# Kernel optimization log

Measured on AMD Instinct MI355X. Metric: run time of the kernel, lower is better.

## Reference

```python
import jax, jax.numpy as jnp
import numpy as np

G = 8          # group (window) size -> N = G*G = 64
HEADS = 8
DIM = 256
HEAD_DIM = DIM // HEADS
SCALE = HEAD_DIM ** -0.5
POS_DIM = (DIM // 4) // 4  # 16
LN_EPS = 1e-5


def _make_bias_tables():
    # biases: coordinates (1-g..g-1) x (1-g..g-1) -> [(2g-1)^2, 2] float
    r = np.arange(1 - G, G)
    bh, bw = np.meshgrid(r, r, indexing='ij')
    biases = np.stack([bh.ravel(), bw.ravel()], axis=1).astype(np.float32)
    # relative position index [g^2, g^2]
    ch, cw = np.meshgrid(np.arange(G), np.arange(G), indexing='ij')
    coords = np.stack([ch.ravel(), cw.ravel()])              # [2, g^2]
    rel = coords[:, :, None] - coords[:, None, :]            # [2, g^2, g^2]
    rel = rel.transpose(1, 2, 0)
    rel[:, :, 0] += G - 1
    rel[:, :, 1] += G - 1
    rel[:, :, 0] *= 2 * G - 1
    rel_idx = rel.sum(-1).astype(np.int32)                   # [g^2, g^2]
    return biases, rel_idx


def setup_inputs() -> dict:
    key = jax.random.key(0)
    ks = jax.random.split(key, 8)
    B, N, C = 2048, G * G, DIM
    biases_np, rel_idx_np = _make_bias_tables()
    s = lambda fan: 1.0 / np.sqrt(fan)
    return {
        'x': jax.random.normal(ks[0], (B, N, C), jnp.float32),
        'qkv_w': jax.random.normal(ks[1], (C, 3 * C), jnp.float32) * s(C),
        'qkv_b': jnp.zeros((3 * C,), jnp.float32),
        'proj_w': jax.random.normal(ks[2], (C, C), jnp.float32) * s(C),
        'proj_b': jnp.zeros((C,), jnp.float32),
        'pos_proj_w': jax.random.normal(ks[3], (2, POS_DIM), jnp.float32) * s(2),
        'pos_proj_b': jnp.zeros((POS_DIM,), jnp.float32),
        'ln1_g': jnp.ones((POS_DIM,), jnp.float32), 'ln1_b': jnp.zeros((POS_DIM,), jnp.float32),
        'fc1_w': jax.random.normal(ks[4], (POS_DIM, POS_DIM), jnp.float32) * s(POS_DIM),
        'fc1_b': jnp.zeros((POS_DIM,), jnp.float32),
        'ln2_g': jnp.ones((POS_DIM,), jnp.float32), 'ln2_b': jnp.zeros((POS_DIM,), jnp.float32),
        'fc2_w': jax.random.normal(ks[5], (POS_DIM, POS_DIM), jnp.float32) * s(POS_DIM),
        'fc2_b': jnp.zeros((POS_DIM,), jnp.float32),
        'ln3_g': jnp.ones((POS_DIM,), jnp.float32), 'ln3_b': jnp.zeros((POS_DIM,), jnp.float32),
        'fc3_w': jax.random.normal(ks[6], (POS_DIM, HEADS), jnp.float32) * s(POS_DIM),
        'fc3_b': jnp.zeros((HEADS,), jnp.float32),
        'biases': jnp.asarray(biases_np),
        'rel_idx': jnp.asarray(rel_idx_np),
    }


def _ln(h, g, b):
    m = jnp.mean(h, -1, keepdims=True)
    v = jnp.mean((h - m) ** 2, -1, keepdims=True)
    return (h - m) * jax.lax.rsqrt(v + LN_EPS) * g + b


def reference(x, qkv_w, qkv_b, proj_w, proj_b,
              pos_proj_w, pos_proj_b,
              ln1_g, ln1_b, fc1_w, fc1_b,
              ln2_g, ln2_b, fc2_w, fc2_b,
              ln3_g, ln3_b, fc3_w, fc3_b,
              biases, rel_idx):
    B, N, C = x.shape
    # dynamic position bias MLP: [(2g-1)^2, 2] -> [(2g-1)^2, heads]
    h = biases @ pos_proj_w + pos_proj_b
    h = jax.nn.relu(_ln(h, ln1_g, ln1_b)) @ fc1_w + fc1_b
    h = jax.nn.relu(_ln(h, ln2_g, ln2_b)) @ fc2_w + fc2_b
    pos = jax.nn.relu(_ln(h, ln3_g, ln3_b)) @ fc3_w + fc3_b        # [225, H]
    rel_bias = pos[rel_idx]                                        # [N, N, H]
    rel_bias = jnp.transpose(rel_bias, (2, 0, 1))                  # [H, N, N]

    qkv = (x @ qkv_w + qkv_b).reshape(B, N, 3, HEADS, HEAD_DIM)
    qkv = jnp.transpose(qkv, (2, 0, 3, 1, 4))                      # [3, B, H, N, Dh]
    q, k, v = qkv[0] * SCALE, qkv[1], qkv[2]
    attn = jnp.einsum('bhnd,bhmd->bhnm', q, k) + rel_bias[None]    # [B, H, N, N]
    attn = jax.nn.softmax(attn, axis=-1)
    out = jnp.einsum('bhnm,bhmd->bhnd', attn, v)                   # [B, H, N, Dh]
    out = jnp.transpose(out, (0, 2, 1, 3)).reshape(B, N, C)
    return out @ proj_w + proj_b
```

## Files before the change

kernel.cpp:

```cpp
#include <hip/hip_runtime.h>

typedef _Float16 half_t;
typedef __attribute__((ext_vector_type(8))) _Float16 half8;
typedef __attribute__((ext_vector_type(4))) _Float16 half4;
typedef __attribute__((ext_vector_type(4))) float float4v;

#define LN_EPS 1e-5f
#define QK_SCALE 0.17677669529663687f

static __device__ __forceinline__ float4v mfma16(half8 a, half8 b, float4v c) {
    return __builtin_amdgcn_mfma_f32_16x16x32_f16(a, b, c, 0, 0, 0);
}

static __device__ __forceinline__ int swzA(int row, int colByte) {
    return row * 512 + ((((colByte >> 4) ^ ((row >> 1) & 7)) << 4) | (colByte & 15));
}
static __device__ __forceinline__ int swzB(int row, int colByte) {
    return row * 64 + ((((colByte >> 4) ^ ((row >> 1) & 3)) << 4) | (colByte & 15));
}
static __device__ __forceinline__ int swzC(int row, int colByte) {
    return row * 128 + ((((colByte >> 4) ^ (row & 7)) << 4) | (colByte & 15));
}

static __device__ void ln_relu16(float* h, const float* __restrict__ g, const float* __restrict__ b) {
    float m = 0.f;
    for (int j = 0; j < 16; ++j) m += h[j];
    m *= (1.0f / 16.0f);
    float v = 0.f;
    for (int j = 0; j < 16; ++j) { float d = h[j] - m; v += d * d; }
    v *= (1.0f / 16.0f);
    float rs = rsqrtf(v + LN_EPS);
    for (int j = 0; j < 16; ++j) {
        float t = (h[j] - m) * rs * g[j] + b[j];
        h[j] = t > 0.f ? t : 0.f;
    }
}

__global__ void prep_kernel(
    const float* __restrict__ qkv_w,
    const float* __restrict__ proj_w,
    const float* __restrict__ biases,
    const float* __restrict__ pos_w, const float* __restrict__ pos_b,
    const float* __restrict__ ln1_g, const float* __restrict__ ln1_b,
    const float* __restrict__ fc1_w, const float* __restrict__ fc1_b,
    const float* __restrict__ ln2_g, const float* __restrict__ ln2_b,
    const float* __restrict__ fc2_w, const float* __restrict__ fc2_b,
    const float* __restrict__ ln3_g, const float* __restrict__ ln3_b,
    const float* __restrict__ fc3_w, const float* __restrict__ fc3_b,
    const int* __restrict__ rel_idx,
    half_t* __restrict__ wqkvT,
    half_t* __restrict__ wprojT,
    float* __restrict__ rbp)
{
    __shared__ float tile[64][65];
    __shared__ float pos_s[225][8];
    const int t = blockIdx.x;
    const int tid = threadIdx.x;

    if (t < 64) {
        const float* src; half_t* dst; int ncols, rg, cg;
        if (t < 48) { src = qkv_w;  dst = wqkvT;  ncols = 768; rg = t / 12;      cg = t % 12; }
        else        { src = proj_w; dst = wprojT; ncols = 256; rg = (t-48) >> 2; cg = (t-48) & 3; }
        const int r0 = tid >> 6, c = tid & 63;
        for (int i = 0; i < 16; ++i) {
            int r = i * 4 + r0;
            tile[r][c] = src[(rg * 64 + r) * ncols + cg * 64 + c];
        }
        __syncthreads();
        for (int i = 0; i < 16; ++i) {
            int r = i * 4 + r0;
            dst[(cg * 64 + r) * 256 + rg * 64 + c] = (half_t)tile[c][r];
        }
    } else {
        if (tid < 225) {
            float h[16], h2[16];
            float b0 = biases[tid * 2], b1 = biases[tid * 2 + 1];
            for (int j = 0; j < 16; ++j) h[j] = b0 * pos_w[j] + b1 * pos_w[16 + j] + pos_b[j];
            ln_relu16(h, ln1_g, ln1_b);
            for (int j = 0; j < 16; ++j) {
                float s = fc1_b[j];
                for (int k = 0; k < 16; ++k) s += h[k] * fc1_w[k * 16 + j];
                h2[j] = s;
            }
            ln_relu16(h2, ln2_g, ln2_b);
            for (int j = 0; j < 16; ++j) {
                float s = fc2_b[j];
                for (int k = 0; k < 16; ++k) s += h2[k] * fc2_w[k * 16 + j];
                h[j] = s;
            }
            ln_relu16(h, ln3_g, ln3_b);
            for (int j = 0; j < 8; ++j) {
                float s = fc3_b[j];
                for (int k = 0; k < 16; ++k) s += h[k] * fc3_w[k * 8 + j];
                pos_s[tid][j] = s;
            }
        }
        __syncthreads();
        for (int e = tid; e < 8 * 64 * 64; e += 256) {
            int hh = e >> 12, rem = e & 4095;
            int row = rem >> 6, c = rem & 63;
            int tj = c >> 4, mm = c & 15;
            rbp[hh * 4096 + row * 64 + mm * 4 + tj] = pos_s[rel_idx[row * 64 + c]][hh];
        }
    }
}

__global__ __launch_bounds__(256, 3) void qkv_attn_kernel(
    const float* __restrict__ x,
    const half_t* __restrict__ wqkvT,
    const float* __restrict__ qkv_b,
    const float* __restrict__ rbp,
    half_t* __restrict__ attn_ws)
{
    __shared__ __align__(16) char smem[49152];
    char* xs = smem;

    const int bb  = blockIdx.x;
    const int win = bb >> 1;
    const int tid = threadIdx.x;
    const int w    = tid >> 6;
    const int h    = (bb & 1) * 4 + w;
    const int lane = tid & 63;
    const int m = lane & 15;
    const int g = lane >> 4;
    char* wA  = smem + 32768 + w * 4096;
    char* vts = xs + w * 8192;

    const float* xg = x + (size_t)win * 16384;
    #pragma unroll
    for (int i = 0; i < 16; ++i) {
        int u = tid + i * 256;
        int row = u >> 6, c4 = u & 63;
        float4v xv = *(const float4v*)(xg + u * 4);
        half4 hv;
        hv[0] = (half_t)xv[0]; hv[1] = (half_t)xv[1];
        hv[2] = (half_t)xv[2]; hv[3] = (half_t)xv[3];
        *(half4*)(xs + swzA(row, c4 * 8)) = hv;
    }
    __syncthreads();

    float4v qb[2][2];
    #pragma unroll
    for (int pt = 0; pt < 2; ++pt)
        #pragma unroll
        for (int c2 = 0; c2 < 2; ++c2)
            qb[pt][c2] = *(const float4v*)(qkv_b + pt * 256 + h * 32 + c2 * 16 + g * 4);

    half8 aq[4], bk[4];
    {
        float4v qa[2][4], ka[2][4];
        #pragma unroll
        for (int c2 = 0; c2 < 2; ++c2)
            #pragma unroll
            for (int ti = 0; ti < 4; ++ti) {
                qa[c2][ti] = {0.f, 0.f, 0.f, 0.f};
                ka[c2][ti] = {0.f, 0.f, 0.f, 0.f};
            }
        const half_t* wqb = wqkvT + (size_t)(h * 32 + m) * 256 + g * 8;
        #pragma unroll
        for (int kk = 0; kk < 8; ++kk) {
            half8 af[4];
            #pragma unroll
            for (int ti = 0; ti < 4; ++ti)
                af[ti] = *(const half8*)(xs + swzA(ti * 16 + m, kk * 64 + g * 16));
            half8 wq0 = *(const half8*)(wqb + kk * 32);
            half8 wq1 = *(const half8*)(wqb + 16 * 256 + kk * 32);
            half8 wk0 = *(const half8*)(wqb + 256 * 256 + kk * 32);
            half8 wk1 = *(const half8*)(wqb + 272 * 256 + kk * 32);
            #pragma unroll
            for (int ti = 0; ti < 4; ++ti) {
                qa[0][ti] = mfma16(wq0, af[ti], qa[0][ti]);
                qa[1][ti] = mfma16(wq1, af[ti], qa[1][ti]);
                ka[0][ti] = mfma16(wk0, af[ti], ka[0][ti]);
                ka[1][ti] = mfma16(wk1, af[ti], ka[1][ti]);
            }
        }
        #pragma unroll
        for (int c2 = 0; c2 < 2; ++c2)
            #pragma unroll
            for (int ti = 0; ti < 4; ++ti) {
                half4 t;
                #pragma unroll
                for (int r = 0; r < 4; ++r) t[r] = (half_t)(qa[c2][ti][r] + qb[0][c2][r]);
                *(half4*)(wA + ti * 1024 + swzB(m, (c2 * 16 + g * 4) * 2)) = t;
            }
        #pragma unroll
        for (int ti = 0; ti < 4; ++ti)
            aq[ti] = *(const half8*)(wA + ti * 1024 + swzB(m, g * 16));
        __builtin_amdgcn_sched_barrier(0);
        #pragma unroll
        for (int c2 = 0; c2 < 2; ++c2)
            #pragma unroll
            for (int ti = 0; ti < 4; ++ti) {
                half4 t;
                #pragma unroll
                for (int r = 0; r < 4; ++r) t[r] = (half_t)(ka[c2][ti][r] + qb[1][c2][r]);
                *(half4*)(wA + ti * 1024 + swzB(m, (c2 * 16 + g * 4) * 2)) = t;
            }
        #pragma unroll
        for (int ti = 0; ti < 4; ++ti)
            bk[ti] = *(const half8*)(wA + ti * 1024 + swzB(m, g * 16));
        __builtin_amdgcn_sched_barrier(0);
    }

    half4 ph[4][4];
    const float* rbh = rbp + h * 4096;
    #pragma unroll
    for (int ti = 0; ti < 4; ++ti) {
        float4v z = {0.f, 0.f, 0.f, 0.f};
        float4v s0 = mfma16(aq[ti], bk[0], z);
        float4v s1 = mfma16(aq[ti], bk[1], z);
        float4v s2 = mfma16(aq[ti], bk[2], z);
        float4v s3 = mfma16(aq[ti], bk[3], z);
        #pragma unroll
        for (int r = 0; r < 4; ++r) {
            float4v rb = *(const float4v*)(rbh + (ti * 16 + g * 4 + r) * 64 + m * 4);
            float e0 = __expf(s0[r] * QK_SCALE + rb[0]);
            float e1 = __expf(s1[r] * QK_SCALE + rb[1]);
            float e2 = __expf(s2[r] * QK_SCALE + rb[2]);
            float e3 = __expf(s3[r] * QK_SCALE + rb[3]);
            float s = e0 + e1 + e2 + e3;
            s += __shfl_xor(s, 1); s += __shfl_xor(s, 2);
            s += __shfl_xor(s, 4); s += __shfl_xor(s, 8);
            float is = 1.0f / s;
            ph[ti][0][r] = (half_t)(e0 * is);
            ph[ti][1][r] = (half_t)(e1 * is);
            ph[ti][2][r] = (half_t)(e2 * is);
            ph[ti][3][r] = (half_t)(e3 * is);
        }
    }

    half4 vh[2][4];
    {
        float4v va[2][4];
        #pragma unroll
        for (int c2 = 0; c2 < 2; ++c2)
            #pragma unroll
            for (int ti = 0; ti < 4; ++ti) va[c2][ti] = {0.f, 0.f, 0.f, 0.f};
        const half_t* wvb = wqkvT + (size_t)(512 + h * 32 + m) * 256 + g * 8;
        #pragma unroll
        for (int kk = 0; kk < 8; ++kk) {
            half8 wv0 = *(const half8*)(wvb + kk * 32);
            half8 wv1 = *(const half8*)(wvb + 16 * 256 + kk * 32);
            #pragma unroll
            for (int ti = 0; ti < 4; ++ti) {
                half8 af = *(const half8*)(xs + swzA(ti * 16 + m, kk * 64 + g * 16));
                va[0][ti] = mfma16(af, wv0, va[0][ti]);
                va[1][ti] = mfma16(af, wv1, va[1][ti]);
            }
        }
        float vb0 = qkv_b[512 + h * 32 + m], vb1 = qkv_b[512 + h * 32 + 16 + m];
        #pragma unroll
        for (int c2 = 0; c2 < 2; ++c2)
            #pragma unroll
            for (int ti = 0; ti < 4; ++ti)
                #pragma unroll
                for (int r = 0; r < 4; ++r)
                    vh[c2][ti][r] = (half_t)(va[c2][ti][r] + (c2 ? vb1 : vb0));
    }
    __syncthreads();

    #pragma unroll
    for (int c2 = 0; c2 < 2; ++c2)
        #pragma unroll
        for (int ti = 0; ti < 4; ++ti)
            *(half4*)(vts + swzC(c2 * 16 + m, ti * 32 + g * 8)) = vh[c2][ti];

    float4v oacc[2][4];
    #pragma unroll
    for (int tjd = 0; tjd < 2; ++tjd)
        #pragma unroll
        for (int ti = 0; ti < 4; ++ti) oacc[tjd][ti] = {0.f, 0.f, 0.f, 0.f};
    #pragma unroll
    for (int nc = 0; nc < 2; ++nc) {
        #pragma unroll
        for (int ti = 0; ti < 4; ++ti)
            #pragma unroll
            for (int t2 = 0; t2 < 2; ++t2)
                #pragma unroll
                for (int r = 0; r < 4; ++r)
                    *(half_t*)(wA + swzB(ti * 16 + g * 4 + r, (t2 * 16 + m) * 2)) =
                        ph[ti][nc * 2 + t2][r];
        half8 pa[4];
        #pragma unroll
        for (int ti = 0; ti < 4; ++ti)
            pa[ti] = *(const half8*)(wA + swzB(ti * 16 + m, g * 16));
        #pragma unroll
        for (int tjd = 0; tjd < 2; ++tjd) {
            half8 bv = *(const half8*)(vts + swzC(tjd * 16 + m, nc * 64 + g * 16));
            #pragma unroll
            for (int ti = 0; ti < 4; ++ti)
                oacc[tjd][ti] = mfma16(pa[ti], bv, oacc[tjd][ti]);
        }
        __builtin_amdgcn_sched_barrier(0);
    }

    half_t* ag = attn_ws + (size_t)win * 16384;
    #pragma unroll
    for (int tjd = 0; tjd < 2; ++tjd)
        #pragma unroll
        for (int ti = 0; ti < 4; ++ti)
            #pragma unroll
            for (int r = 0; r < 4; ++r)
                ag[(ti * 16 + g * 4 + r) * 256 + h * 32 + tjd * 16 + m] =
                    (half_t)oacc[tjd][ti][r];
}

__global__ __launch_bounds__(256, 4) void proj_kernel(
    const half_t* __restrict__ attn_ws,
    const half_t* __restrict__ wprojT,
    const float* __restrict__ proj_b,
    float* __restrict__ out)
{
    __shared__ __align__(16) char smem[32768];
    char* xs = smem;

    const int win = blockIdx.x;
    const int tid = threadIdx.x;
    const int w    = tid >> 6;
    const int lane = tid & 63;
    const int m = lane & 15;
    const int g = lane >> 4;

    const half_t* ag = attn_ws + (size_t)win * 16384;
    #pragma unroll
    for (int i = 0; i < 8; ++i) {
        int u = tid + i * 256;
        int row = u >> 5, c8 = u & 31;
        half8 v = *(const half8*)(ag + u * 8);
        *(half8*)(xs + swzA(row, c8 * 16)) = v;
    }
    __syncthreads();

    float* og = out + (size_t)win * 16384;
    #pragma unroll
    for (int cp = 0; cp < 2; ++cp) {
        const int oc0 = w * 64 + cp * 32;
        float4v pacc[2][4];
        #pragma unroll
        for (int c2 = 0; c2 < 2; ++c2)
            #pragma unroll
            for (int ti = 0; ti < 4; ++ti) pacc[c2][ti] = {0.f, 0.f, 0.f, 0.f};
        const half_t* wpb = wprojT + (size_t)(oc0 + m) * 256 + g * 8;
        #pragma unroll
        for (int kk = 0; kk < 8; ++kk) {
            half8 wf0 = *(const half8*)(wpb + kk * 32);
            half8 wf1 = *(const half8*)(wpb + 16 * 256 + kk * 32);
            #pragma unroll
            for (int ti = 0; ti < 4; ++ti) {
                half8 af = *(const half8*)(xs + swzA(ti * 16 + m, kk * 64 + g * 16));
                pacc[0][ti] = mfma16(af, wf0, pacc[0][ti]);
                pacc[1][ti] = mfma16(af, wf1, pacc[1][ti]);
            }
        }
        float pb0 = proj_b[oc0 + m], pb1 = proj_b[oc0 + 16 + m];
        #pragma unroll
        for (int c2 = 0; c2 < 2; ++c2)
            #pragma unroll
            for (int ti = 0; ti < 4; ++ti)
                #pragma unroll
                for (int r = 0; r < 4; ++r)
                    og[(ti * 16 + g * 4 + r) * 256 + oc0 + c2 * 16 + m] =
                        pacc[c2][ti][r] + (c2 ? pb1 : pb0);
    }
}

__global__ __launch_bounds__(512, 2) void fused_fallback(
    const float* __restrict__ x,
    const half_t* __restrict__ wqkvT,
    const float* __restrict__ qkv_b,
    const half_t* __restrict__ wprojT,
    const float* __restrict__ proj_b,
    const float* __restrict__ rbp,
    float* __restrict__ out)
{
    __shared__ __align__(16) char smem[65536];
    char* xs  = smem;
    char* atn = smem;
    char* arenas = smem + 32768;

    const int b   = blockIdx.x;
    const int tid = threadIdx.x;
    const int w    = tid >> 6;
    const int lane = tid & 63;
    const int m = lane & 15;
    const int g = lane >> 4;
    char* wA  = arenas + w * 4096;
    char* vts = xs + w * 4096;

    const float* xg = x + (size_t)b * 16384;
    #pragma unroll
    for (int i = 0; i < 8; ++i) {
        int u = tid + i * 512;
        int row = u >> 6, c4 = u & 63;
        float4v xv = *(const float4v*)(xg + u * 4);
        half4 hv;
        hv[0] = (half_t)xv[0]; hv[1] = (half_t)xv[1];
        hv[2] = (half_t)xv[2]; hv[3] = (half_t)xv[3];
        *(half4*)(xs + swzA(row, c4 * 8)) = hv;
    }
    __syncthreads();

    float4v qb[2][2];
    #pragma unroll
    for (int pt = 0; pt < 2; ++pt)
        #pragma unroll
        for (int c2 = 0; c2 < 2; ++c2)
            qb[pt][c2] = *(const float4v*)(qkv_b + pt * 256 + w * 32 + c2 * 16 + g * 4);

    half8 aq[4], bk[4];
    {
        float4v qa[2][4], ka[2][4];
        #pragma unroll
        for (int c2 = 0; c2 < 2; ++c2)
            #pragma unroll
            for (int ti = 0; ti < 4; ++ti) {
                qa[c2][ti] = {0.f, 0.f, 0.f, 0.f};
                ka[c2][ti] = {0.f, 0.f, 0.f, 0.f};
            }
        const half_t* wqb = wqkvT + (size_t)(w * 32 + m) * 256 + g * 8;
        #pragma unroll
        for (int kk = 0; kk < 8; ++kk) {
            half8 af[4];
            #pragma unroll
            for (int ti = 0; ti < 4; ++ti)
                af[ti] = *(const half8*)(xs + swzA(ti * 16 + m, kk * 64 + g * 16));
            half8 wq0 = *(const half8*)(wqb + kk * 32);
            half8 wq1 = *(const half8*)(wqb + 16 * 256 + kk * 32);
            half8 wk0 = *(const half8*)(wqb + 256 * 256 + kk * 32);
            half8 wk1 = *(const half8*)(wqb + 272 * 256 + kk * 32);
            #pragma unroll
            for (int ti = 0; ti < 4; ++ti) {
                qa[0][ti] = mfma16(wq0, af[ti], qa[0][ti]);
                qa[1][ti] = mfma16(wq1, af[ti], qa[1][ti]);
                ka[0][ti] = mfma16(wk0, af[ti], ka[0][ti]);
                ka[1][ti] = mfma16(wk1, af[ti], ka[1][ti]);
            }
        }
        #pragma unroll
        for (int c2 = 0; c2 < 2; ++c2)
            #pragma unroll
            for (int ti = 0; ti < 4; ++ti) {
                half4 t;
                #pragma unroll
                for (int r = 0; r < 4; ++r) t[r] = (half_t)(qa[c2][ti][r] + qb[0][c2][r]);
                *(half4*)(wA + ti * 1024 + swzB(m, (c2 * 16 + g * 4) * 2)) = t;
            }
        #pragma unroll
        for (int ti = 0; ti < 4; ++ti)
            aq[ti] = *(const half8*)(wA + ti * 1024 + swzB(m, g * 16));
        __builtin_amdgcn_sched_barrier(0);
        #pragma unroll
        for (int c2 = 0; c2 < 2; ++c2)
            #pragma unroll
            for (int ti = 0; ti < 4; ++ti) {
                half4 t;
                #pragma unroll
                for (int r = 0; r < 4; ++r) t[r] = (half_t)(ka[c2][ti][r] + qb[1][c2][r]);
                *(half4*)(wA + ti * 1024 + swzB(m, (c2 * 16 + g * 4) * 2)) = t;
            }
        #pragma unroll
        for (int ti = 0; ti < 4; ++ti)
            bk[ti] = *(const half8*)(wA + ti * 1024 + swzB(m, g * 16));
        __builtin_amdgcn_sched_barrier(0);
    }

    half4 ph[4][4];
    const float* rbh = rbp + w * 4096;
    #pragma unroll
    for (int ti = 0; ti < 4; ++ti) {
        float4v z = {0.f, 0.f, 0.f, 0.f};
        float4v s0 = mfma16(aq[ti], bk[0], z);
        float4v s1 = mfma16(aq[ti], bk[1], z);
        float4v s2 = mfma16(aq[ti], bk[2], z);
        float4v s3 = mfma16(aq[ti], bk[3], z);
        #pragma unroll
        for (int r = 0; r < 4; ++r) {
            float4v rb = *(const float4v*)(rbh + (ti * 16 + g * 4 + r) * 64 + m * 4);
            float e0 = __expf(s0[r] * QK_SCALE + rb[0]);
            float e1 = __expf(s1[r] * QK_SCALE + rb[1]);
            float e2 = __expf(s2[r] * QK_SCALE + rb[2]);
            float e3 = __expf(s3[r] * QK_SCALE + rb[3]);
            float s = e0 + e1 + e2 + e3;
            s += __shfl_xor(s, 1); s += __shfl_xor(s, 2);
            s += __shfl_xor(s, 4); s += __shfl_xor(s, 8);
            float is = 1.0f / s;
            ph[ti][0][r] = (half_t)(e0 * is);
            ph[ti][1][r] = (half_t)(e1 * is);
            ph[ti][2][r] = (half_t)(e2 * is);
            ph[ti][3][r] = (half_t)(e3 * is);
        }
    }

    half4 vh[2][4];
    {
        float4v va[2][4];
        #pragma unroll
        for (int c2 = 0; c2 < 2; ++c2)
            #pragma unroll
            for (int ti = 0; ti < 4; ++ti) va[c2][ti] = {0.f, 0.f, 0.f, 0.f};
        const half_t* wvb = wqkvT + (size_t)(512 + w * 32 + m) * 256 + g * 8;
        #pragma unroll
        for (int kk = 0; kk < 8; ++kk) {
            half8 wv0 = *(const half8*)(wvb + kk * 32);
            half8 wv1 = *(const half8*)(wvb + 16 * 256 + kk * 32);
            #pragma unroll
            for (int ti = 0; ti < 4; ++ti) {
                half8 af = *(const half8*)(xs + swzA(ti * 16 + m, kk * 64 + g * 16));
                va[0][ti] = mfma16(af, wv0, va[0][ti]);
                va[1][ti] = mfma16(af, wv1, va[1][ti]);
            }
        }
        float vb0 = qkv_b[512 + w * 32 + m], vb1 = qkv_b[512 + w * 32 + 16 + m];
        #pragma unroll
        for (int c2 = 0; c2 < 2; ++c2)
            #pragma unroll
            for (int ti = 0; ti < 4; ++ti)
                #pragma unroll
                for (int r = 0; r < 4; ++r)
                    vh[c2][ti][r] = (half_t)(va[c2][ti][r] + (c2 ? vb1 : vb0));
    }
    __syncthreads();

    #pragma unroll
    for (int c2 = 0; c2 < 2; ++c2)
        #pragma unroll
        for (int ti = 0; ti < 4; ++ti)
            *(half4*)(vts + swzC(c2 * 16 + m, ti * 32 + g * 8)) = vh[c2][ti];

    float4v oacc[2][4];
    #pragma unroll
    for (int tjd = 0; tjd < 2; ++tjd)
        #pragma unroll
        for (int ti = 0; ti < 4; ++ti) oacc[tjd][ti] = {0.f, 0.f, 0.f, 0.f};
    #pragma unroll
    for (int nc = 0; nc < 2; ++nc) {
        #pragma unroll
        for (int ti = 0; ti < 4; ++ti)
            #pragma unroll
            for (int t2 = 0; t2 < 2; ++t2)
                #pragma unroll
                for (int r = 0; r < 4; ++r)
                    *(half_t*)(wA + swzB(ti * 16 + g * 4 + r, (t2 * 16 + m) * 2)) =
                        ph[ti][nc * 2 + t2][r];
        half8 pa[4];
        #pragma unroll
        for (int ti = 0; ti < 4; ++ti)
            pa[ti] = *(const half8*)(wA + swzB(ti * 16 + m, g * 16));
        #pragma unroll
        for (int tjd = 0; tjd < 2; ++tjd) {
            half8 bv = *(const half8*)(vts + swzC(tjd * 16 + m, nc * 64 + g * 16));
            #pragma unroll
            for (int ti = 0; ti < 4; ++ti)
                oacc[tjd][ti] = mfma16(pa[ti], bv, oacc[tjd][ti]);
        }
        __builtin_amdgcn_sched_barrier(0);
    }
    __syncthreads();

    #pragma unroll
    for (int tjd = 0; tjd < 2; ++tjd)
        #pragma unroll
        for (int ti = 0; ti < 4; ++ti)
            #pragma unroll
            for (int r = 0; r < 4; ++r)
                *(half_t*)(atn + swzA(ti * 16 + g * 4 + r, (w * 32 + tjd * 16 + m) * 2)) =
                    (half_t)oacc[tjd][ti][r];
    __syncthreads();

    float* og = out + (size_t)b * 16384;
    const int oc0 = w * 32;
    float4v pacc[2][4];
    #pragma unroll
    for (int c2 = 0; c2 < 2; ++c2)
        #pragma unroll
        for (int ti = 0; ti < 4; ++ti) pacc[c2][ti] = {0.f, 0.f, 0.f, 0.f};
    const half_t* wpb = wprojT + (size_t)(oc0 + m) * 256 + g * 8;
    #pragma unroll
    for (int kk = 0; kk < 8; ++kk) {
        half8 wf0 = *(const half8*)(wpb + kk * 32);
        half8 wf1 = *(const half8*)(wpb + 16 * 256 + kk * 32);
        #pragma unroll
        for (int ti = 0; ti < 4; ++ti) {
            half8 af = *(const half8*)(atn + swzA(ti * 16 + m, kk * 64 + g * 16));
            pacc[0][ti] = mfma16(af, wf0, pacc[0][ti]);
            pacc[1][ti] = mfma16(af, wf1, pacc[1][ti]);
        }
    }
    float pb0 = proj_b[oc0 + m], pb1 = proj_b[oc0 + 16 + m];
    #pragma unroll
    for (int c2 = 0; c2 < 2; ++c2)
        #pragma unroll
        for (int ti = 0; ti < 4; ++ti)
            #pragma unroll
            for (int r = 0; r < 4; ++r)
                og[(ti * 16 + g * 4 + r) * 256 + oc0 + c2 * 16 + m] =
                    pacc[c2][ti][r] + (c2 ? pb1 : pb0);
}

extern "C" void kernel_launch(void* const* d_in, const int* in_sizes, int n_in,
                              void* d_out, int out_size, void* d_ws, size_t ws_size,
                              hipStream_t stream) {
    const float* x          = (const float*)d_in[0];
    const float* qkv_w      = (const float*)d_in[1];
    const float* qkv_b      = (const float*)d_in[2];
    const float* proj_w     = (const float*)d_in[3];
    const float* proj_b     = (const float*)d_in[4];
    const float* pos_proj_w = (const float*)d_in[5];
    const float* pos_proj_b = (const float*)d_in[6];
    const float* ln1_g = (const float*)d_in[7];
    const float* ln1_b = (const float*)d_in[8];
    const float* fc1_w = (const float*)d_in[9];
    const float* fc1_b = (const float*)d_in[10];
    const float* ln2_g = (const float*)d_in[11];
    const float* ln2_b = (const float*)d_in[12];
    const float* fc2_w = (const float*)d_in[13];
    const float* fc2_b = (const float*)d_in[14];
    const float* ln3_g = (const float*)d_in[15];
    const float* ln3_b = (const float*)d_in[16];
    const float* fc3_w = (const float*)d_in[17];
    const float* fc3_b = (const float*)d_in[18];
    const float* biases = (const float*)d_in[19];
    const int*  rel_idx = (const int*)d_in[20];

    half_t* wqkvT  = (half_t*)d_ws;
    half_t* wprojT = (half_t*)((char*)d_ws + 393216);
    float*  rbp    = (float*)((char*)d_ws + 524288);
    half_t* attn_ws = (half_t*)((char*)d_ws + 655360);

    const int B = in_sizes[0] / (64 * 256);
    const size_t need = 655360 + (size_t)B * 64 * 256 * 2;

    prep_kernel<<<65, 256, 0, stream>>>(qkv_w, proj_w, biases, pos_proj_w, pos_proj_b,
                                        ln1_g, ln1_b, fc1_w, fc1_b,
                                        ln2_g, ln2_b, fc2_w, fc2_b,
                                        ln3_g, ln3_b, fc3_w, fc3_b,
                                        rel_idx, wqkvT, wprojT, rbp);
    if (ws_size >= need) {
        qkv_attn_kernel<<<B * 2, 256, 0, stream>>>(x, wqkvT, qkv_b, rbp, attn_ws);
        proj_kernel<<<B, 256, 0, stream>>>(attn_ws, wprojT, proj_b, (float*)d_out);
    } else {
        fused_fallback<<<B, 512, 0, stream>>>(x, wqkvT, qkv_b, wprojT, proj_b, rbp,
                                              (float*)d_out);
    }
}
```

Measured before the change: 311.5 us.

## Split fused QKV+attention into separate QKV GEMM and attention kernels

Replaces the per-head fused QKV projection and attention kernel with a per-window QKV GEMM kernel, which writes Q, K and transposed V to global scratch, followed by a separate attention kernel. The goal is to stop loading and converting x twice per window and to give the GEMM better occupancy. In exchange, Q, K and V make extra round trips through global memory, d_out is reused as temporary storage, and a larger workspace is required.

```diff
diff --git a/kernel.cpp b/kernel.cpp
--- a/kernel.cpp
+++ b/kernel.cpp
@@ -105,26 +105,19 @@
     }
 }
 
-__global__ __launch_bounds__(256, 3) void qkv_attn_kernel(
+__global__ __launch_bounds__(256, 4) void qkv_gemm_kernel(
     const float* __restrict__ x,
     const half_t* __restrict__ wqkvT,
     const float* __restrict__ qkv_b,
-    const float* __restrict__ rbp,
-    half_t* __restrict__ attn_ws)
+    half_t* __restrict__ q_ws,
+    half_t* __restrict__ k_ws,
+    half_t* __restrict__ vt_ws)
 {
-    __shared__ __align__(16) char smem[49152];
+    __shared__ __align__(16) char smem[32768];
     char* xs = smem;
-
-    const int bb  = blockIdx.x;
-    const int win = bb >> 1;
+    const int win = blockIdx.x;
     const int tid = threadIdx.x;
-    const int w    = tid >> 6;
-    const int h    = (bb & 1) * 4 + w;
-    const int lane = tid & 63;
-    const int m = lane & 15;
-    const int g = lane >> 4;
-    char* wA  = smem + 32768 + w * 4096;
-    char* vts = xs + w * 8192;
+    const int w = tid >> 6, lane = tid & 63, m = lane & 15, g = lane >> 4;
 
     const float* xg = x + (size_t)win * 16384;
     #pragma unroll
@@ -139,71 +132,81 @@
     }
     __syncthreads();
 
-    float4v qb[2][2];
-    #pragma unroll
-    for (int pt = 0; pt < 2; ++pt)
-        #pragma unroll
-        for (int c2 = 0; c2 < 2; ++c2)
-            qb[pt][c2] = *(const float4v*)(qkv_b + pt * 256 + h * 32 + c2 * 16 + g * 4);
-
-    half8 aq[4], bk[4];
-    {
-        float4v qa[2][4], ka[2][4];
-        #pragma unroll
-        for (int c2 = 0; c2 < 2; ++c2)
-            #pragma unroll
-            for (int ti = 0; ti < 4; ++ti) {
-                qa[c2][ti] = {0.f, 0.f, 0.f, 0.f};
-                ka[c2][ti] = {0.f, 0.f, 0.f, 0.f};
-            }
-        const half_t* wqb = wqkvT + (size_t)(h * 32 + m) * 256 + g * 8;
+    #pragma unroll
+    for (int p = 0; p < 6; ++p) {
+        const int ct0 = w * 12 + p * 2;
+        float4v acc[2][4];
+        #pragma unroll
+        for (int c2 = 0; c2 < 2; ++c2)
+            #pragma unroll
+            for (int ti = 0; ti < 4; ++ti) acc[c2][ti] = {0.f, 0.f, 0.f, 0.f};
+        const half_t* wb = wqkvT + (size_t)(ct0 * 16 + m) * 256 + g * 8;
         #pragma unroll
         for (int kk = 0; kk < 8; ++kk) {
             half8 af[4];
             #pragma unroll
             for (int ti = 0; ti < 4; ++ti)
                 af[ti] = *(const half8*)(xs + swzA(ti * 16 + m, kk * 64 + g * 16));
-            half8 wq0 = *(const half8*)(wqb + kk * 32);
-            half8 wq1 = *(const half8*)(wqb + 16 * 256 + kk * 32);
-            half8 wk0 = *(const half8*)(wqb + 256 * 256 + kk * 32);
-            half8 wk1 = *(const half8*)(wqb + 272 * 256 + kk * 32);
+            half8 wf0 = *(const half8*)(wb + kk * 32);
+            half8 wf1 = *(const half8*)(wb + 16 * 256 + kk * 32);
             #pragma unroll
             for (int ti = 0; ti < 4; ++ti) {
-                qa[0][ti] = mfma16(wq0, af[ti], qa[0][ti]);
-                qa[1][ti] = mfma16(wq1, af[ti], qa[1][ti]);
-                ka[0][ti] = mfma16(wk0, af[ti], ka[0][ti]);
-                ka[1][ti] = mfma16(wk1, af[ti], ka[1][ti]);
-            }
-        }
-        #pragma unroll
-        for (int c2 = 0; c2 < 2; ++c2)
-            #pragma unroll
-            for (int ti = 0; ti < 4; ++ti) {
-                half4 t;
+                acc[0][ti] = mfma16(af[ti], wf0, acc[0][ti]);
+                acc[1][ti] = mfma16(af[ti], wf1, acc[1][ti]);
+            }
+        }
+        #pragma unroll
+        for (int c2 = 0; c2 < 2; ++c2) {
+            const int ct = ct0 + c2;
+            const float bias = qkv_b[ct * 16 + m];
+            if (ct < 32) {
+                half_t* dst = (ct < 16 ? q_ws : k_ws)
+                              + (size_t)win * 16384 + (ct & 15) * 16 + m;
                 #pragma unroll
-                for (int r = 0; r < 4; ++r) t[r] = (half_t)(qa[c2][ti][r] + qb[0][c2][r]);
-                *(half4*)(wA + ti * 1024 + swzB(m, (c2 * 16 + g * 4) * 2)) = t;
-            }
-        #pragma unroll
-        for (int ti = 0; ti < 4; ++ti)
-            aq[ti] = *(const half8*)(wA + ti * 1024 + swzB(m, g * 16));
-        __builtin_amdgcn_sched_barrier(0);
-        #pragma unroll
-        for (int c2 = 0; c2 < 2; ++c2)
-            #pragma unroll
-            for (int ti = 0; ti < 4; ++ti) {
-                half4 t;
+                for (int ti = 0; ti < 4; ++ti)
+                    #pragma unroll
+                    for (int r = 0; r < 4; ++r)
+                        dst[(size_t)(ti * 16 + g * 4 + r) * 256] =
+                            (half_t)(acc[c2][ti][r] + bias);
+            } else {
+                const int c = (ct - 32) * 16 + m;
+                const int h = c >> 5, dm = c & 31;
+                half_t* vd = vt_ws + ((size_t)(win * 8 + h) * 32 + dm) * 64;
                 #pragma unroll
-                for (int r = 0; r < 4; ++r) t[r] = (half_t)(ka[c2][ti][r] + qb[1][c2][r]);
-                *(half4*)(wA + ti * 1024 + swzB(m, (c2 * 16 + g * 4) * 2)) = t;
-            }
-        #pragma unroll
-        for (int ti = 0; ti < 4; ++ti)
-            bk[ti] = *(const half8*)(wA + ti * 1024 + swzB(m, g * 16));
-        __builtin_amdgcn_sched_barrier(0);
-    }
-
-    half4 ph[4][4];
+                for (int ti = 0; ti < 4; ++ti) {
+                    half4 pk;
+                    #pragma unroll
+                    for (int r = 0; r < 4; ++r) pk[r] = (half_t)(acc[c2][ti][r] + bias);
+                    *(half4*)(vd + ti * 16 + g * 4) = pk;
+                }
+            }
+        }
+    }
+}
+
+__global__ __launch_bounds__(256, 3) void attn_kernel(
+    const half_t* __restrict__ q_ws,
+    const half_t* __restrict__ k_ws,
+    const half_t* __restrict__ vt_ws,
+    const float* __restrict__ rbp,
+    half_t* __restrict__ attn_ws)
+{
+    __shared__ __align__(16) char smem[32768];
+    const int bb = blockIdx.x, win = bb >> 1;
+    const int tid = threadIdx.x;
+    const int w = tid >> 6, lane = tid & 63, m = lane & 15, g = lane >> 4;
+    const int h = (bb & 1) * 4 + w;
+    char* wP = smem + w * 8192;
+
+    const half_t* qb_ = q_ws + (size_t)win * 16384 + h * 32 + g * 8;
+    const half_t* kb_ = k_ws + (size_t)win * 16384 + h * 32 + g * 8;
+    half8 aq[4], bk[4];
+    #pragma unroll
+    for (int t = 0; t < 4; ++t) {
+        aq[t] = *(const half8*)(qb_ + (size_t)(t * 16 + m) * 256);
+        bk[t] = *(const half8*)(kb_ + (size_t)(t * 16 + m) * 256);
+    }
+
     const float* rbh = rbp + h * 4096;
     #pragma unroll
     for (int ti = 0; ti < 4; ++ti) {
@@ -214,7 +217,8 @@
         float4v s3 = mfma16(aq[ti], bk[3], z);
         #pragma unroll
         for (int r = 0; r < 4; ++r) {
-            float4v rb = *(const float4v*)(rbh + (ti * 16 + g * 4 + r) * 64 + m * 4);
+            const int row = ti * 16 + g * 4 + r;
+            float4v rb = *(const float4v*)(rbh + row * 64 + m * 4);
             float e0 = __expf(s0[r] * QK_SCALE + rb[0]);
             float e1 = __expf(s1[r] * QK_SCALE + rb[1]);
             float e2 = __expf(s2[r] * QK_SCALE + rb[2]);
@@ -223,76 +227,32 @@
             s += __shfl_xor(s, 1); s += __shfl_xor(s, 2);
             s += __shfl_xor(s, 4); s += __shfl_xor(s, 8);
             float is = 1.0f / s;
-            ph[ti][0][r] = (half_t)(e0 * is);
-            ph[ti][1][r] = (half_t)(e1 * is);
-            ph[ti][2][r] = (half_t)(e2 * is);
-            ph[ti][3][r] = (half_t)(e3 * is);
-        }
-    }
-
-    half4 vh[2][4];
-    {
-        float4v va[2][4];
-        #pragma unroll
-        for (int c2 = 0; c2 < 2; ++c2)
-            #pragma unroll
-            for (int ti = 0; ti < 4; ++ti) va[c2][ti] = {0.f, 0.f, 0.f, 0.f};
-        const half_t* wvb = wqkvT + (size_t)(512 + h * 32 + m) * 256 + g * 8;
-        #pragma unroll
-        for (int kk = 0; kk < 8; ++kk) {
-            half8 wv0 = *(const half8*)(wvb + kk * 32);
-            half8 wv1 = *(const half8*)(wvb + 16 * 256 + kk * 32);
-            #pragma unroll
-            for (int ti = 0; ti < 4; ++ti) {
-                half8 af = *(const half8*)(xs + swzA(ti * 16 + m, kk * 64 + g * 16));
-                va[0][ti] = mfma16(af, wv0, va[0][ti]);
-                va[1][ti] = mfma16(af, wv1, va[1][ti]);
-            }
-        }
-        float vb0 = qkv_b[512 + h * 32 + m], vb1 = qkv_b[512 + h * 32 + 16 + m];
-        #pragma unroll
-        for (int c2 = 0; c2 < 2; ++c2)
-            #pragma unroll
-            for (int ti = 0; ti < 4; ++ti)
-                #pragma unroll
-                for (int r = 0; r < 4; ++r)
-                    vh[c2][ti][r] = (half_t)(va[c2][ti][r] + (c2 ? vb1 : vb0));
-    }
-    __syncthreads();
-
-    #pragma unroll
-    for (int c2 = 0; c2 < 2; ++c2)
-        #pragma unroll
-        for (int ti = 0; ti < 4; ++ti)
-            *(half4*)(vts + swzC(c2 * 16 + m, ti * 32 + g * 8)) = vh[c2][ti];
+            *(half_t*)(wP + swzC(row, (m) * 2))       = (half_t)(e0 * is);
+            *(half_t*)(wP + swzC(row, (16 + m) * 2))  = (half_t)(e1 * is);
+            *(half_t*)(wP + swzC(row, (32 + m) * 2))  = (half_t)(e2 * is);
+            *(half_t*)(wP + swzC(row, (48 + m) * 2))  = (half_t)(e3 * is);
+        }
+    }
 
     float4v oacc[2][4];
     #pragma unroll
     for (int tjd = 0; tjd < 2; ++tjd)
         #pragma unroll
         for (int ti = 0; ti < 4; ++ti) oacc[tjd][ti] = {0.f, 0.f, 0.f, 0.f};
-    #pragma unroll
-    for (int nc = 0; nc < 2; ++nc) {
-        #pragma unroll
-        for (int ti = 0; ti < 4; ++ti)
-            #pragma unroll
-            for (int t2 = 0; t2 < 2; ++t2)
-                #pragma unroll
-                for (int r = 0; r < 4; ++r)
-                    *(half_t*)(wA + swzB(ti * 16 + g * 4 + r, (t2 * 16 + m) * 2)) =
-                        ph[ti][nc * 2 + t2][r];
+    const half_t* vb_ = vt_ws + (size_t)(win * 8 + h) * 2048 + g * 8;
+    #pragma unroll
+    for (int kc = 0; kc < 2; ++kc) {
         half8 pa[4];
         #pragma unroll
         for (int ti = 0; ti < 4; ++ti)
-            pa[ti] = *(const half8*)(wA + swzB(ti * 16 + m, g * 16));
+            pa[ti] = *(const half8*)(wP + swzC(ti * 16 + m, kc * 64 + g * 16));
         #pragma unroll
         for (int tjd = 0; tjd < 2; ++tjd) {
-            half8 bv = *(const half8*)(vts + swzC(tjd * 16 + m, nc * 64 + g * 16));
+            half8 bv = *(const half8*)(vb_ + (tjd * 16 + m) * 64 + kc * 32);
             #pragma unroll
             for (int ti = 0; ti < 4; ++ti)
                 oacc[tjd][ti] = mfma16(pa[ti], bv, oacc[tjd][ti]);
         }
-        __builtin_amdgcn_sched_barrier(0);
     }
 
     half_t* ag = attn_ws + (size_t)win * 16384;
@@ -302,7 +262,7 @@
         for (int ti = 0; ti < 4; ++ti)
             #pragma unroll
             for (int r = 0; r < 4; ++r)
-                ag[(ti * 16 + g * 4 + r) * 256 + h * 32 + tjd * 16 + m] =
+                ag[(size_t)(ti * 16 + g * 4 + r) * 256 + h * 32 + tjd * 16 + m] =
                     (half_t)oacc[tjd][ti][r];
 }
 
@@ -317,10 +277,7 @@
 
     const int win = blockIdx.x;
     const int tid = threadIdx.x;
-    const int w    = tid >> 6;
-    const int lane = tid & 63;
-    const int m = lane & 15;
-    const int g = lane >> 4;
+    const int w = tid >> 6, lane = tid & 63, m = lane & 15, g = lane >> 4;
 
     const half_t* ag = attn_ws + (size_t)win * 16384;
     #pragma unroll
@@ -626,10 +583,13 @@
     half_t* wqkvT  = (half_t*)d_ws;
     half_t* wprojT = (half_t*)((char*)d_ws + 393216);
     float*  rbp    = (float*)((char*)d_ws + 524288);
-    half_t* attn_ws = (half_t*)((char*)d_ws + 655360);
 
     const int B = in_sizes[0] / (64 * 256);
-    const size_t need = 655360 + (size_t)B * 64 * 256 * 2;
+    half_t* q_ws    = (half_t*)d_out;
+    half_t* k_ws    = q_ws + (size_t)B * 16384;
+    half_t* vt_ws   = (half_t*)((char*)d_ws + 655360);
+    half_t* attn_ws = vt_ws + (size_t)B * 16384;
+    const size_t need = 655360 + (size_t)B * 65536;
 
     prep_kernel<<<65, 256, 0, stream>>>(qkv_w, proj_w, biases, pos_proj_w, pos_proj_b,
                                         ln1_g, ln1_b, fc1_w, fc1_b,
@@ -637,7 +597,8 @@
                                         ln3_g, ln3_b, fc3_w, fc3_b,
                                         rel_idx, wqkvT, wprojT, rbp);
     if (ws_size >= need) {
-        qkv_attn_kernel<<<B * 2, 256, 0, stream>>>(x, wqkvT, qkv_b, rbp, attn_ws);
+        qkv_gemm_kernel<<<B, 256, 0, stream>>>(x, wqkvT, qkv_b, q_ws, k_ws, vt_ws);
+        attn_kernel<<<B * 2, 256, 0, stream>>>(q_ws, k_ws, vt_ws, rbp, attn_ws);
         proj_kernel<<<B, 256, 0, stream>>>(attn_ws, wprojT, proj_b, (float*)d_out);
     } else {
         fused_fallback<<<B, 512, 0, stream>>>(x, wqkvT, qkv_b, wprojT, proj_b, rbp,
```

Result: slower. 394.3 us (+26.6%).
